# Kernel tuning notes

Measured on AMD Instinct MI355X. Metric: run time of the kernel, lower is better.

Reference implementation:

```python
import jax, jax.numpy as jnp
import numpy as np

B, C, O, H, W, K = 4, 64, 64, 128, 128, 3
K2 = K * K


def setup_inputs() -> dict:
    key = jax.random.key(0)
    ks = jax.random.split(key, 11)
    def n(k, shape, scale=0.05):
        return jax.random.normal(k, shape, jnp.float32) * scale
    return dict(
        x=jax.random.normal(ks[0], (B, C, H, W), jnp.float32),
        eps=jax.random.normal(ks[1], (B, 2 * K2, H, W), jnp.float32),
        w_fc1=n(ks[2], (2 * K2, C, K, K)), b_fc1=n(ks[3], (2 * K2,)),
        w_fc2=n(ks[4], (2 * K2, C, K, K)), b_fc2=n(ks[5], (2 * K2,)),
        w_off=n(ks[6], (2 * K2, C, K, K)), b_off=n(ks[7], (2 * K2,)),
        w_mod=n(ks[8], (K2, C, K, K)), b_mod=n(ks[9], (K2,)),
        w_reg=n(ks[10], (O, C, K, K)),
    )


def conv2d(x, w, b):
    # 3x3, stride 1, padding 1 (SAME), NCHW/OIHW
    y = jax.lax.conv_general_dilated(
        x, w, window_strides=(1, 1), padding=((1, 1), (1, 1)),
        dimension_numbers=('NCHW', 'OIHW', 'NCHW'))
    return y + b[None, :, None, None]


def deform_conv2d(x, offset, mask, weight):
    # torchvision.ops.deform_conv2d semantics: offset [B, 2*K2, H, W] with
    # (dy, dx) pairs per kernel position, zero-padded bilinear sampling.
    Bn, Cn, Hn, Wn = x.shape
    off = offset.reshape(Bn, K2, 2, Hn, Wn)
    ky = jnp.arange(K2) // K  # kernel row per tap
    kx = jnp.arange(K2) % K   # kernel col per tap
    # base sampling grid: h*stride - pad + k (stride=1, pad=1)
    base_y = jnp.arange(Hn)[None, :, None] + (ky - 1)[:, None, None]  # [K2,H,W]
    base_x = jnp.arange(Wn)[None, None, :] + (kx - 1)[:, None, None]
    py = base_y[None].astype(jnp.float32) + off[:, :, 0]  # [B,K2,H,W]
    px = base_x[None].astype(jnp.float32) + off[:, :, 1]

    def sample_one(xb, pyb, pxb):  # xb [C,H,W]; pyb/pxb [K2,H,W]
        y0 = jnp.floor(pyb)
        x0 = jnp.floor(pxb)
        ly = pyb - y0
        lx = pxb - x0
        y0i = y0.astype(jnp.int32)
        x0i = x0.astype(jnp.int32)

        def g(yi, xi, wgt):
            valid = (yi >= 0) & (yi < Hn) & (xi >= 0) & (xi < Wn)
            v = xb[:, jnp.clip(yi, 0, Hn - 1), jnp.clip(xi, 0, Wn - 1)]  # [C,K2,H,W]
            return v * (wgt * valid)[None]

        return (g(y0i, x0i, (1 - ly) * (1 - lx))
                + g(y0i, x0i + 1, (1 - ly) * lx)
                + g(y0i + 1, x0i, ly * (1 - lx))
                + g(y0i + 1, x0i + 1, ly * lx))

    sampled = jax.vmap(sample_one)(x, py, px)  # [B,C,K2,H,W]
    sampled = sampled * mask[:, None]          # modulation
    w2 = weight.reshape(weight.shape[0], Cn, K2)
    return jnp.einsum('bckhw,ock->bohw', sampled, w2)


def reference(x, eps, w_fc1, b_fc1, w_fc2, b_fc2, w_off, b_off, w_mod, b_mod, w_reg):
    # VAE branch: mu/log_var via relu convs, reparameterize, sigmoid gate
    mu = jax.nn.relu(conv2d(x, w_fc1, b_fc1))
    log_var = jax.nn.relu(conv2d(x, w_fc2, b_fc2))
    z = eps * jnp.exp(0.5 * log_var) + mu
    gate = jax.nn.sigmoid(z)
    # gated offsets + modulation mask
    offset = conv2d(x, w_off, b_off) * gate
    modulator = 2.0 * jax.nn.sigmoid(conv2d(x, w_mod, b_mod))
    return deform_conv2d(x, offset, modulator, w_reg)
```

## Files before the change

### kernel.cpp

```cpp
#include <hip/hip_runtime.h>

typedef __attribute__((ext_vector_type(8))) __bf16 bf16x8;
typedef __attribute__((ext_vector_type(4))) float f32x4;
typedef unsigned short ushortT;

#define Bn 4
#define Hn 128
#define Wn 128
#define HP 130
#define WP 130
#define HW (Hn * Wn)

#define XP_ELEMS (Bn * HP * WP * 64)
#define WCAT_ELEMS (64 * 576)

__device__ __forceinline__ ushortT f2bf_u(float f) {
    unsigned int u = __float_as_uint(f);
    return (ushortT)((u + 0x8000u) >> 16);
}

__global__ __launch_bounds__(256) void prep4(
    const float* __restrict__ x,
    const float* __restrict__ w1, const float* __restrict__ w2,
    const float* __restrict__ wo, const float* __restrict__ wm,
    const float* __restrict__ wr,
    ushortT* __restrict__ xp, ushortT* __restrict__ wcatF, ushortT* __restrict__ wregF)
{
    __shared__ float tl[64][69];
    int blk = blockIdx.x;
    int tid = threadIdx.x;

    if (blk < 1024) {
        int b = blk >> 8;
        int chunk = blk & 255;
        int hw0 = chunk << 6;
        int y = hw0 >> 7;
        int w0 = hw0 & 127;
        const float* xb = x + (size_t)b * 64 * HW + hw0;
        for (int i = tid; i < 4096; i += 256) {
            int c = i >> 6, w = i & 63;
            tl[w][c] = xb[(size_t)c * HW + w];
        }
        __syncthreads();
        uint2* dst = (uint2*)(xp + ((size_t)(b * HP + y + 1) * WP + (w0 + 1)) * 64);
        for (int j = tid; j < 1024; j += 256) {
            int w = j >> 4, cp = j & 15;
            uint2 u;
            u.x = (uint)f2bf_u(tl[w][4 * cp])     | ((uint)f2bf_u(tl[w][4 * cp + 1]) << 16);
            u.y = (uint)f2bf_u(tl[w][4 * cp + 2]) | ((uint)f2bf_u(tl[w][4 * cp + 3]) << 16);
            dst[j] = u;
        }
    } else if (blk < 1152) {
        int idx = (blk - 1024) * 256 + tid;
        if (idx < 16512) {
            int b, y, w, e;
            if (idx < 8320) {
                int p = idx >> 3; e = idx & 7;
                b = p / 260; int rr = p - b * 260;
                y = (rr < 130) ? 0 : (HP - 1);
                w = (rr < 130) ? rr : (rr - 130);
            } else {
                int g = idx - 8320;
                int p = g >> 3; e = g & 7;
                b = p >> 8; int rr = p & 255;
                y = 1 + (rr & 127);
                w = (rr < 128) ? 0 : (WP - 1);
            }
            uint4 z = {0u, 0u, 0u, 0u};
            ((uint4*)xp)[((size_t)(b * HP + y) * WP + w) * 8 + e] = z;
        }
    } else if (blk < 1296) {
        int t = (blk - 1152) * 256 + tid;
        int frag = t >> 9;
        int rem = t & 511;
        int l = rem >> 3, j = rem & 7;
        int kpos = frag >> 3;
        int ks = (frag >> 2) & 1;
        int mt = frag & 3;
        int ch = mt * 16 + (l & 15);
        int c = ks * 32 + (l >> 4) * 8 + j;
        float v = 0.f;
        if (ch < 18)      v = w1[(ch * 64 + c) * 9 + kpos];
        else if (ch < 36) v = w2[((ch - 18) * 64 + c) * 9 + kpos];
        else if (ch < 54) v = wo[((ch - 36) * 64 + c) * 9 + kpos];
        else if (ch < 63) v = wm[((ch - 54) * 64 + c) * 9 + kpos];
        wcatF[t] = f2bf_u(v);
    } else {
        int t = (blk - 1296) * 256 + tid;
        int frag = t >> 9;
        int rem = t & 511;
        int l = rem >> 3, j = rem & 7;
        int kpos = frag >> 3;
        int ks = (frag >> 2) & 1;
        int mt = frag & 3;
        int o = mt * 16 + (l & 15);
        int c = ks * 32 + (l >> 4) * 8 + j;
        wregF[t] = f2bf_u(wr[(o * 64 + c) * 9 + kpos]);
    }
}

__global__ __launch_bounds__(256, 2) void fusedP(
    const ushortT* __restrict__ xp, const float* __restrict__ eps,
    const float* __restrict__ b1, const float* __restrict__ b2,
    const float* __restrict__ bo, const float* __restrict__ bm,
    const ushortT* __restrict__ wcatF, const ushortT* __restrict__ wregF,
    float* __restrict__ out)
{
    __shared__ float  Cls[128 * 65];
    __shared__ int4   cOffL[9 * 128];
    __shared__ float4 cWgtL[9 * 128];

    int bid = blockIdx.x;
    int blk = (bid & 7) * 64 + (bid >> 3);
    int h = blk & 127;
    int b = blk >> 7;
    int tid = threadIdx.x;
    int l = tid & 63;
    int wv = tid >> 6;
    int lane15 = l & 15;
    int g4 = l >> 4;
    int kl8 = g4 << 3;
    int p0 = wv << 5;

    const bf16x8* WcF = (const bf16x8*)wcatF;
    const bf16x8* WrF = (const bf16x8*)wregF;

    const f32x4 zero4 = {0.f, 0.f, 0.f, 0.f};
    f32x4 acc[4][2];
#pragma unroll
    for (int mt = 0; mt < 4; ++mt) { acc[mt][0] = zero4; acc[mt][1] = zero4; }

#pragma unroll
    for (int kpos = 0; kpos < 9; ++kpos) {
        const int ky = kpos / 3, kx = kpos % 3;
        const ushortT* xrow = xp + (size_t)(b * HP + h + ky) * (WP * 64);

        bf16x8 afr[4][2];
#pragma unroll
        for (int mt = 0; mt < 4; ++mt)
#pragma unroll
            for (int ks = 0; ks < 2; ++ks)
                afr[mt][ks] = WcF[(size_t)((kpos * 2 + ks) * 4 + mt) * 64 + l];

        bf16x8 bfr[2][2];
#pragma unroll
        for (int nt = 0; nt < 2; ++nt) {
            const ushortT* bp = xrow + (size_t)(p0 + nt * 16 + lane15 + kx) * 64 + kl8;
#pragma unroll
            for (int ks = 0; ks < 2; ++ks)
                bfr[nt][ks] = *(const bf16x8*)(bp + ks * 32);
        }

#pragma unroll
        for (int nt = 0; nt < 2; ++nt)
#pragma unroll
            for (int ks = 0; ks < 2; ++ks)
#pragma unroll
                for (int mt = 0; mt < 4; ++mt)
                    acc[mt][nt] = __builtin_amdgcn_mfma_f32_16x16x32_bf16(afr[mt][ks], bfr[nt][ks], acc[mt][nt], 0, 0, 0);
    }

#pragma unroll
    for (int nt = 0; nt < 2; ++nt)
#pragma unroll
        for (int mt = 0; mt < 4; ++mt)
#pragma unroll
            for (int r = 0; r < 4; ++r)
                Cls[(p0 + nt * 16 + lane15) * 65 + mt * 16 + g4 * 4 + r] = acc[mt][nt][r];
    __syncthreads();

#pragma unroll
    for (int kk = 0; kk < 5; ++kk) {
        int item = kk * 256 + tid;
        if (item < 1152) {
            int k = item >> 7;
            int pix = item & 127;
            int ky = k / 3, kx = k % 3;
            const float* crow = Cls + pix * 65;
            float offv[2];
#pragma unroll
            for (int d = 0; d < 2; ++d) {
                int ch = 2 * k + d;
                float mu = fmaxf(crow[ch] + b1[ch], 0.f);
                float lv = fmaxf(crow[18 + ch] + b2[ch], 0.f);
                float e  = eps[((size_t)(b * 18 + ch) * Hn + h) * Wn + pix];
                float z  = fmaf(e, __expf(0.5f * lv), mu);
                float gate = 1.f / (1.f + __expf(-z));
                offv[d] = (crow[36 + ch] + bo[ch]) * gate;
            }
            float m = 2.f / (1.f + __expf(-(crow[54 + k] + bm[k])));
            float py = (float)(h + ky - 1) + offv[0];
            float px = (float)(pix + kx - 1) + offv[1];
            float y0f = floorf(py), x0f = floorf(px);
            float ly = py - y0f, lx = px - x0f;
            int y0 = (int)y0f, x0 = (int)x0f;
            int y1 = y0 + 1, x1 = x0 + 1;
            bool okY0 = (y0 >= 0) & (y0 < Hn);
            bool okY1 = (y1 >= 0) & (y1 < Hn);
            bool okX0 = (x0 >= 0) & (x0 < Wn);
            bool okX1 = (x1 >= 0) & (x1 < Wn);
            int y0c = min(max(y0, 0), Hn - 1) + 1, y1c = min(max(y1, 0), Hn - 1) + 1;
            int x0c = min(max(x0, 0), Wn - 1) + 1, x1c = min(max(x1, 0), Wn - 1) + 1;
            int rb = b * HP;
            int4 co;
            co.x = ((rb + y0c) * WP + x0c) * 64;
            co.y = ((rb + y0c) * WP + x1c) * 64;
            co.z = ((rb + y1c) * WP + x0c) * 64;
            co.w = ((rb + y1c) * WP + x1c) * 64;
            float4 wq;
            wq.x = (1.f - ly) * (1.f - lx) * ((okY0 & okX0) ? m : 0.f);
            wq.y = (1.f - ly) * lx         * ((okY0 & okX1) ? m : 0.f);
            wq.z = ly * (1.f - lx)         * ((okY1 & okX0) ? m : 0.f);
            wq.w = ly * lx                 * ((okY1 & okX1) ? m : 0.f);
            cOffL[k * 128 + pix] = co;
            cWgtL[k * 128 + pix] = wq;
        }
    }
    __syncthreads();

    f32x4 dcc[4][2];
#pragma unroll
    for (int mt = 0; mt < 4; ++mt) { dcc[mt][0] = zero4; dcc[mt][1] = zero4; }

#pragma unroll
    for (int kpos = 0; kpos < 9; ++kpos) {
        bf16x8 afr[4][2];
#pragma unroll
        for (int mt = 0; mt < 4; ++mt)
#pragma unroll
            for (int ks = 0; ks < 2; ++ks)
                afr[mt][ks] = WrF[(size_t)((kpos * 2 + ks) * 4 + mt) * 64 + l];

#pragma unroll
        for (int nt = 0; nt < 2; ++nt) {
            int pix = p0 + nt * 16 + lane15;
            int4 co   = cOffL[kpos * 128 + pix];
            float4 wq = cWgtL[kpos * 128 + pix];
            bf16x8 v00[2], v01[2], v10[2], v11[2];
#pragma unroll
            for (int ks = 0; ks < 2; ++ks) {
                int cofs = ks * 32 + kl8;
                v00[ks] = *(const bf16x8*)(xp + co.x + cofs);
                v01[ks] = *(const bf16x8*)(xp + co.y + cofs);
                v10[ks] = *(const bf16x8*)(xp + co.z + cofs);
                v11[ks] = *(const bf16x8*)(xp + co.w + cofs);
            }
#pragma unroll
            for (int ks = 0; ks < 2; ++ks) {
                bf16x8 bfr;
#pragma unroll
                for (int j = 0; j < 8; ++j) {
                    float f = wq.x * (float)v00[ks][j];
                    f = fmaf(wq.y, (float)v01[ks][j], f);
                    f = fmaf(wq.z, (float)v10[ks][j], f);
                    f = fmaf(wq.w, (float)v11[ks][j], f);
                    bfr[j] = (__bf16)f;
                }
#pragma unroll
                for (int mt = 0; mt < 4; ++mt)
                    dcc[mt][nt] = __builtin_amdgcn_mfma_f32_16x16x32_bf16(afr[mt][ks], bfr, dcc[mt][nt], 0, 0, 0);
            }
        }
    }

#pragma unroll
    for (int nt = 0; nt < 2; ++nt)
#pragma unroll
        for (int mt = 0; mt < 4; ++mt)
#pragma unroll
            for (int r = 0; r < 4; ++r) {
                int o = mt * 16 + g4 * 4 + r;
                out[((size_t)(b * 64 + o) * Hn + h) * Wn + p0 + nt * 16 + lane15] = dcc[mt][nt][r];
            }
}

extern "C" void kernel_launch(void* const* d_in, const int* in_sizes, int n_in,
                              void* d_out, int out_size, void* d_ws, size_t ws_size,
                              hipStream_t stream) {
    const float* x     = (const float*)d_in[0];
    const float* eps   = (const float*)d_in[1];
    const float* w_fc1 = (const float*)d_in[2];
    const float* b_fc1 = (const float*)d_in[3];
    const float* w_fc2 = (const float*)d_in[4];
    const float* b_fc2 = (const float*)d_in[5];
    const float* w_off = (const float*)d_in[6];
    const float* b_off = (const float*)d_in[7];
    const float* w_mod = (const float*)d_in[8];
    const float* b_mod = (const float*)d_in[9];
    const float* w_reg = (const float*)d_in[10];

    ushortT* xp    = (ushortT*)d_ws;
    ushortT* wcatF = xp + XP_ELEMS;
    ushortT* wregF = wcatF + WCAT_ELEMS;

    prep4<<<1440, 256, 0, stream>>>(x, w_fc1, w_fc2, w_off, w_mod, w_reg,
                                    xp, wcatF, wregF);
    fusedP<<<512, 256, 0, stream>>>(xp, eps, b_fc1, b_fc2, b_off, b_mod,
                                    wcatF, wregF, (float*)d_out);
}
```

Before: 144.3 us.

## Stage padded input row tile in LDS for conv and deformable gather

Each block first copies six padded input rows (130 columns × 64 bf16 channels, padded stride) into shared memory. Both the regular 3x3 convolution B-fragment loads and the bilinear gathers then read from this tile. Gathers whose sample row falls outside the tile fall back to global memory, signalled by negative offsets. LDS use grows to about 150 KB, so occupancy drops to one block per CU via launch bounds. Cls reads are staged into registers before the offset and weight buffers overwrite that aliased region.

```diff
diff --git a/kernel.cpp b/kernel.cpp
--- a/kernel.cpp
+++ b/kernel.cpp
@@ -13,6 +13,12 @@
 
 #define XP_ELEMS (Bn * HP * WP * 64)
 #define WCAT_ELEMS (64 * 576)
+
+#define TROWS 6
+#define TCOLS 130
+#define CSTRIDE 144
+#define TILE_BYTES (TROWS * TCOLS * CSTRIDE)
+#define U2_BYTES (9 * 128 * 32)
 
 __device__ __forceinline__ ushortT f2bf_u(float f) {
     unsigned int u = __float_as_uint(f);
@@ -99,16 +105,18 @@
     }
 }
 
-__global__ __launch_bounds__(256, 2) void fusedP(
+__global__ __launch_bounds__(256, 1) void fusedQ(
     const ushortT* __restrict__ xp, const float* __restrict__ eps,
     const float* __restrict__ b1, const float* __restrict__ b2,
     const float* __restrict__ bo, const float* __restrict__ bm,
     const ushortT* __restrict__ wcatF, const ushortT* __restrict__ wregF,
     float* __restrict__ out)
 {
-    __shared__ float  Cls[128 * 65];
-    __shared__ int4   cOffL[9 * 128];
-    __shared__ float4 cWgtL[9 * 128];
+    __shared__ __align__(16) char SH[TILE_BYTES + U2_BYTES];
+    char*   tile  = SH;
+    int4*   cOffL = (int4*)(SH + TILE_BYTES);
+    float4* cWgtL = (float4*)(SH + TILE_BYTES + 9 * 128 * 16);
+    float*  Cls   = (float*)(SH + TILE_BYTES);
 
     int bid = blockIdx.x;
     int blk = (bid & 7) * 64 + (bid >> 3);
@@ -125,6 +133,20 @@
     const bf16x8* WcF = (const bf16x8*)wcatF;
     const bf16x8* WrF = (const bf16x8*)wregF;
 
+#pragma unroll
+    for (int i = 0; i < TROWS; ++i) {
+        int ypad = h - 1 + i;
+        if (ypad >= 0 && ypad <= 129) {
+            const uint4* srow = (const uint4*)(xp + ((size_t)(b * HP + ypad) * WP) * 64);
+            char* drow = tile + i * (TCOLS * CSTRIDE);
+            for (int t2 = tid; t2 < TCOLS * 8; t2 += 256) {
+                int cj = t2 >> 3, sub = t2 & 7;
+                *(uint4*)(drow + cj * CSTRIDE + sub * 16) = srow[cj * 8 + sub];
+            }
+        }
+    }
+    __syncthreads();
+
     const f32x4 zero4 = {0.f, 0.f, 0.f, 0.f};
     f32x4 acc[4][2];
 #pragma unroll
@@ -133,7 +155,6 @@
 #pragma unroll
     for (int kpos = 0; kpos < 9; ++kpos) {
         const int ky = kpos / 3, kx = kpos % 3;
-        const ushortT* xrow = xp + (size_t)(b * HP + h + ky) * (WP * 64);
 
         bf16x8 afr[4][2];
 #pragma unroll
@@ -145,10 +166,10 @@
         bf16x8 bfr[2][2];
 #pragma unroll
         for (int nt = 0; nt < 2; ++nt) {
-            const ushortT* bp = xrow + (size_t)(p0 + nt * 16 + lane15 + kx) * 64 + kl8;
-#pragma unroll
-            for (int ks = 0; ks < 2; ++ks)
-                bfr[nt][ks] = *(const bf16x8*)(bp + ks * 32);
+            int cell = (ky + 1) * TCOLS + (p0 + nt * 16 + lane15 + kx);
+            const char* bp = tile + cell * CSTRIDE + g4 * 16;
+            bfr[nt][0] = *(const bf16x8*)(bp);
+            bfr[nt][1] = *(const bf16x8*)(bp + 64);
         }
 
 #pragma unroll
@@ -167,6 +188,28 @@
 #pragma unroll
             for (int r = 0; r < 4; ++r)
                 Cls[(p0 + nt * 16 + lane15) * 65 + mt * 16 + g4 * 4 + r] = acc[mt][nt][r];
+    __syncthreads();
+
+    float rA[5][7];
+    float eA[5][2];
+#pragma unroll
+    for (int kk = 0; kk < 5; ++kk) {
+        int item = kk * 256 + tid;
+        if (item < 1152) {
+            int k = item >> 7;
+            int pix = item & 127;
+            const float* crow = Cls + pix * 65;
+            rA[kk][0] = crow[2 * k];
+            rA[kk][1] = crow[2 * k + 1];
+            rA[kk][2] = crow[18 + 2 * k];
+            rA[kk][3] = crow[19 + 2 * k];
+            rA[kk][4] = crow[36 + 2 * k];
+            rA[kk][5] = crow[37 + 2 * k];
+            rA[kk][6] = crow[54 + k];
+            eA[kk][0] = eps[((size_t)(b * 18 + 2 * k) * Hn + h) * Wn + pix];
+            eA[kk][1] = eps[((size_t)(b * 18 + 2 * k + 1) * Hn + h) * Wn + pix];
+        }
+    }
     __syncthreads();
 
 #pragma unroll
@@ -176,19 +219,17 @@
             int k = item >> 7;
             int pix = item & 127;
             int ky = k / 3, kx = k % 3;
-            const float* crow = Cls + pix * 65;
             float offv[2];
 #pragma unroll
             for (int d = 0; d < 2; ++d) {
                 int ch = 2 * k + d;
-                float mu = fmaxf(crow[ch] + b1[ch], 0.f);
-                float lv = fmaxf(crow[18 + ch] + b2[ch], 0.f);
-                float e  = eps[((size_t)(b * 18 + ch) * Hn + h) * Wn + pix];
-                float z  = fmaf(e, __expf(0.5f * lv), mu);
+                float mu = fmaxf(rA[kk][d] + b1[ch], 0.f);
+                float lv = fmaxf(rA[kk][2 + d] + b2[ch], 0.f);
+                float z  = fmaf(eA[kk][d], __expf(0.5f * lv), mu);
                 float gate = 1.f / (1.f + __expf(-z));
-                offv[d] = (crow[36 + ch] + bo[ch]) * gate;
-            }
-            float m = 2.f / (1.f + __expf(-(crow[54 + k] + bm[k])));
+                offv[d] = (rA[kk][4 + d] + bo[ch]) * gate;
+            }
+            float m = 2.f / (1.f + __expf(-(rA[kk][6] + bm[k])));
             float py = (float)(h + ky - 1) + offv[0];
             float px = (float)(pix + kx - 1) + offv[1];
             float y0f = floorf(py), x0f = floorf(px);
@@ -202,11 +243,15 @@
             int y0c = min(max(y0, 0), Hn - 1) + 1, y1c = min(max(y1, 0), Hn - 1) + 1;
             int x0c = min(max(x0, 0), Wn - 1) + 1, x1c = min(max(x1, 0), Wn - 1) + 1;
             int rb = b * HP;
+            int iy0 = y0c - (h - 1);
+            int iy1 = y1c - (h - 1);
+            bool in0 = (iy0 >= 0) & (iy0 < TROWS);
+            bool in1 = (iy1 >= 0) & (iy1 < TROWS);
             int4 co;
-            co.x = ((rb + y0c) * WP + x0c) * 64;
-            co.y = ((rb + y0c) * WP + x1c) * 64;
-            co.z = ((rb + y1c) * WP + x0c) * 64;
-            co.w = ((rb + y1c) * WP + x1c) * 64;
+            co.x = in0 ? (iy0 * TCOLS + x0c) * CSTRIDE : -(((rb + y0c) * WP + x0c) * 64);
+            co.y = in0 ? (iy0 * TCOLS + x1c) * CSTRIDE : -(((rb + y0c) * WP + x1c) * 64);
+            co.z = in1 ? (iy1 * TCOLS + x0c) * CSTRIDE : -(((rb + y1c) * WP + x0c) * 64);
+            co.w = in1 ? (iy1 * TCOLS + x1c) * CSTRIDE : -(((rb + y1c) * WP + x1c) * 64);
             float4 wq;
             wq.x = (1.f - ly) * (1.f - lx) * ((okY0 & okX0) ? m : 0.f);
             wq.y = (1.f - ly) * lx         * ((okY0 & okX1) ? m : 0.f);
@@ -222,6 +267,8 @@
 #pragma unroll
     for (int mt = 0; mt < 4; ++mt) { dcc[mt][0] = zero4; dcc[mt][1] = zero4; }
 
+    int lofs = g4 * 16;
+
 #pragma unroll
     for (int kpos = 0; kpos < 9; ++kpos) {
         bf16x8 afr[4][2];
@@ -237,13 +284,30 @@
             int4 co   = cOffL[kpos * 128 + pix];
             float4 wq = cWgtL[kpos * 128 + pix];
             bf16x8 v00[2], v01[2], v10[2], v11[2];
-#pragma unroll
-            for (int ks = 0; ks < 2; ++ks) {
-                int cofs = ks * 32 + kl8;
-                v00[ks] = *(const bf16x8*)(xp + co.x + cofs);
-                v01[ks] = *(const bf16x8*)(xp + co.y + cofs);
-                v10[ks] = *(const bf16x8*)(xp + co.z + cofs);
-                v11[ks] = *(const bf16x8*)(xp + co.w + cofs);
+            int m4 = min(min(co.x, co.y), min(co.z, co.w));
+            if (__all(m4 >= 0)) {
+#pragma unroll
+                for (int ks = 0; ks < 2; ++ks) {
+                    int o2 = lofs + ks * 64;
+                    v00[ks] = *(const bf16x8*)(tile + co.x + o2);
+                    v01[ks] = *(const bf16x8*)(tile + co.y + o2);
+                    v10[ks] = *(const bf16x8*)(tile + co.z + o2);
+                    v11[ks] = *(const bf16x8*)(tile + co.w + o2);
+                }
+            } else {
+#pragma unroll
+                for (int ks = 0; ks < 2; ++ks) {
+                    int o2 = lofs + ks * 64;
+                    int cofs = ks * 32 + kl8;
+                    if (co.x >= 0) v00[ks] = *(const bf16x8*)(tile + co.x + o2);
+                    else           v00[ks] = *(const bf16x8*)(xp + (-co.x) + cofs);
+                    if (co.y >= 0) v01[ks] = *(const bf16x8*)(tile + co.y + o2);
+                    else           v01[ks] = *(const bf16x8*)(xp + (-co.y) + cofs);
+                    if (co.z >= 0) v10[ks] = *(const bf16x8*)(tile + co.z + o2);
+                    else           v10[ks] = *(const bf16x8*)(xp + (-co.z) + cofs);
+                    if (co.w >= 0) v11[ks] = *(const bf16x8*)(tile + co.w + o2);
+                    else           v11[ks] = *(const bf16x8*)(xp + (-co.w) + cofs);
+                }
             }
 #pragma unroll
             for (int ks = 0; ks < 2; ++ks) {
@@ -295,6 +359,6 @@
 
     prep4<<<1440, 256, 0, stream>>>(x, w_fc1, w_fc2, w_off, w_mod, w_reg,
                                     xp, wcatF, wregF);
-    fusedP<<<512, 256, 0, stream>>>(xp, eps, b_fc1, b_fc2, b_off, b_mod,
+    fusedQ<<<512, 256, 0, stream>>>(xp, eps, b_fc1, b_fc2, b_off, b_mod,
                                     wcatF, wregF, (float*)d_out);
 }
```

After: 143.4 us. Within noise of the previous version (-0.6%).
